# Performance work log

Measured on AMD Instinct MI355X. Metric: run time of the kernel, lower is better.

Reference implementation:

```python
import jax, jax.numpy as jnp
import numpy as np

BS, N, D, NE, NREL = 32, 512, 768, 64, 7


def setup_inputs() -> dict:
    key = jax.random.key(0)
    ks = jax.random.split(key, 8)
    bert_encoded = jax.random.normal(ks[0], (BS, N, D), dtype=jnp.float32)
    # variable-length spans [u, v) with 1 <= v-u <= 8, v <= N
    starts = jax.random.randint(ks[1], (BS, NE), 0, N - 8)
    lengths = jax.random.randint(ks[2], (BS, NE), 1, 9)
    ent_spans = jnp.stack([starts, starts + lengths], axis=-1).astype(jnp.int64)
    # some entities are padding (mask = 0), as in the original ne = max(len)
    ent_mask = (jax.random.uniform(ks[3], (BS, NE)) > 0.2).astype(jnp.float32)
    xav = (2.0 / (D + D)) ** 0.5  # xavier_normal std for square layers
    wq_w = jax.random.normal(ks[4], (D, D), dtype=jnp.float32) * xav
    wk_w = jax.random.normal(ks[5], (D, D), dtype=jnp.float32) * xav
    ln1_w = jax.random.normal(ks[6], (D, D), dtype=jnp.float32) * xav
    lno_w = jax.random.normal(ks[7], (NREL, D), dtype=jnp.float32) * (2.0 / (D + NREL)) ** 0.5
    return {
        "bert_encoded": bert_encoded,
        "ent_spans": ent_spans,
        "ent_mask": ent_mask,
        "wq_w": wq_w, "wq_b": jnp.zeros((D,), jnp.float32),
        "wk_w": wk_w, "wk_b": jnp.zeros((D,), jnp.float32),
        "ln1_w": ln1_w, "ln1_b": jnp.zeros((D,), jnp.float32),
        "lno_w": lno_w, "lno_b": jnp.zeros((NREL,), jnp.float32),
    }


def reference(bert_encoded, ent_spans, ent_mask,
              wq_w, wq_b, wk_w, wk_b, ln1_w, ln1_b, lno_w, lno_b):
    bs, n, d = bert_encoded.shape
    # span mean-pooling via exclusive-cumsum difference: mean over [u, v)
    cs = jnp.concatenate(
        [jnp.zeros((bs, 1, d), bert_encoded.dtype), jnp.cumsum(bert_encoded, axis=1)],
        axis=1)  # [bs, n+1, d]
    u = ent_spans[..., 0]  # [bs, ne]
    v = ent_spans[..., 1]
    cs_u = jnp.take_along_axis(cs, u[:, :, None], axis=1)  # [bs, ne, d]
    cs_v = jnp.take_along_axis(cs, v[:, :, None], axis=1)
    span_len = (v - u).astype(bert_encoded.dtype)[:, :, None]
    ent_encode = (cs_v - cs_u) / span_len
    # padded entities are zero vectors in the original (never written)
    ent_encode = ent_encode * ent_mask[:, :, None]
    # biaffine-style pairwise head (dropout = 0)
    q = jnp.einsum('bed,fd->bef', ent_encode, wq_w) + wq_b  # [bs, ne, d]
    k = jnp.einsum('bed,fd->bef', ent_encode, wk_w) + wk_b
    alpha = jax.nn.relu(q[:, :, None, :] + k[:, None, :, :])  # [bs, ne, ne, d]
    alpha = jax.nn.relu(jnp.einsum('bijd,ed->bije', alpha, ln1_w) + ln1_b)
    alpha = jnp.einsum('bijd,rd->bijr', alpha, lno_w) + lno_b  # [bs, ne, ne, nrel]
    alpha = alpha * ent_mask[:, :, None, None] * ent_mask[:, None, :, None]
    return alpha
```

## Files before the change

### kernel.cpp

```cpp
#include <hip/hip_runtime.h>
#include <hip/hip_bf16.h>

#define D 768
#define NE 64
#define BSZ 32
#define SEQ 512
#define NREL 7
#define NPAIR 131072
#define NEB 6

typedef __attribute__((ext_vector_type(8))) short short8;
typedef __attribute__((ext_vector_type(4))) float floatx4;

__device__ __forceinline__ short f2bf(float x) {
  union { __hip_bfloat16 b; short s; } u;
  u.b = __float2bfloat16(x);
  return u.s;
}

__device__ __forceinline__ float bf2f(short s) {
  return __uint_as_float(((unsigned)(unsigned short)s) << 16);
}

__device__ __forceinline__ void gl_lds16(const void* g, void* l) {
  __builtin_amdgcn_global_load_lds(
      (const __attribute__((address_space(1))) void*)g,
      (__attribute__((address_space(3))) void*)l, 16, 0, 0);
}

__global__ void __launch_bounds__(256) k_convert(const float* wq, const float* wk, const float* ln1,
                                                 short* owq, short* owk, short* oln1) {
  int idx = (blockIdx.x * 256 + threadIdx.x) * 4;
  if (idx >= D * D) return;
  float4 a = *(const float4*)(wq + idx);
  float4 b = *(const float4*)(wk + idx);
  float4 c = *(const float4*)(ln1 + idx);
  owq[idx + 0] = f2bf(a.x); owq[idx + 1] = f2bf(a.y); owq[idx + 2] = f2bf(a.z); owq[idx + 3] = f2bf(a.w);
  owk[idx + 0] = f2bf(b.x); owk[idx + 1] = f2bf(b.y); owk[idx + 2] = f2bf(b.z); owk[idx + 3] = f2bf(b.w);
  oln1[idx + 0] = f2bf(c.x); oln1[idx + 1] = f2bf(c.y); oln1[idx + 2] = f2bf(c.z); oln1[idx + 3] = f2bf(c.w);
}

__global__ void __launch_bounds__(256) k_pool(const float* bert, const int* spans, const float* mask,
                                              short* entb) {
  int be = blockIdx.x;
  int b = be >> 6;
  int u = spans[be * 2], v = spans[be * 2 + 1];
  float scale = mask[be] / (float)(v - u);
  const float* base = bert + (size_t)b * SEQ * D;
  for (int d = threadIdx.x; d < D; d += 256) {
    float s = 0.f;
    for (int t = u; t < v; ++t) s += base[t * D + d];
    entb[(size_t)be * D + d] = f2bf(s * scale);
  }
}

__global__ void __launch_bounds__(256) k_qk(const short* entb, const short* wqb, const short* wkb,
                                            const float* qbias, const float* kbias,
                                            short* qo, short* ko) {
  const int mblk = blockIdx.x, nblk = blockIdx.y;
  const short* W = blockIdx.z ? wkb : wqb;
  const float* bias = blockIdx.z ? kbias : qbias;
  short* out = blockIdx.z ? ko : qo;
  __shared__ __align__(16) char lds[32768];
  const int tid = threadIdx.x, wid = tid >> 6, lane = tid & 63;
  const int wm = wid >> 1, wn = wid & 1;
  floatx4 acc[4][4] = {};
  const int m0 = mblk * 128, n0 = nblk * 128;
  for (int kt = 0; kt < 12; ++kt) {
    const int d0 = kt * 64;
    __syncthreads();
#pragma unroll
    for (int is = 0; is < 4; ++is) {
      int lin = (wid * 4 + is) * 64 + lane;
      int row = lin >> 3, slot = lin & 7;
      int cg = slot ^ (row & 7);
      gl_lds16(entb + (size_t)(m0 + row) * D + d0 + cg * 8, lds + lin * 16);
    }
#pragma unroll
    for (int is = 0; is < 4; ++is) {
      int lin = (wid * 4 + is) * 64 + lane;
      int row = lin >> 3, slot = lin & 7;
      int cg = slot ^ (row & 7);
      gl_lds16(W + (size_t)(n0 + row) * D + d0 + cg * 8, lds + 16384 + lin * 16);
    }
    __syncthreads();
#pragma unroll
    for (int ks = 0; ks < 2; ++ks) {
      int kc = ks * 4 + (lane >> 4);
      short8 af[4], bf_[4];
#pragma unroll
      for (int m = 0; m < 4; ++m) {
        int row = wm * 64 + m * 16 + (lane & 15);
        af[m] = *(const short8*)(lds + row * 128 + ((kc ^ (row & 7)) << 4));
      }
#pragma unroll
      for (int n = 0; n < 4; ++n) {
        int row = wn * 64 + n * 16 + (lane & 15);
        bf_[n] = *(const short8*)(lds + 16384 + row * 128 + ((kc ^ (row & 7)) << 4));
      }
#pragma unroll
      for (int m = 0; m < 4; ++m)
#pragma unroll
        for (int n = 0; n < 4; ++n)
          acc[m][n] = __builtin_amdgcn_mfma_f32_16x16x32_bf16(af[m], bf_[n], acc[m][n], 0, 0, 0);
    }
  }
#pragma unroll
  for (int m = 0; m < 4; ++m)
#pragma unroll
    for (int rg = 0; rg < 4; ++rg) {
      int r = m0 + wm * 64 + m * 16 + ((lane >> 4) << 2) + rg;
#pragma unroll
      for (int n = 0; n < 4; ++n) {
        int c = n0 + wn * 64 + n * 16 + (lane & 15);
        out[(size_t)r * D + c] = f2bf(acc[m][n][rg] + bias[c]);
      }
    }
}

__global__ void __launch_bounds__(256, 3) k_main(const short* w1b, const short* qb, const short* kb,
                                                 const float* l1bias, const float* lno_w,
                                                 float* partial) {
  const int pblk = blockIdx.x, eblk = blockIdx.y;
  const int p0 = pblk * 128, e0 = eblk * 128;
  const int b = p0 >> 12, i0 = (p0 >> 6) & 63;
  __shared__ __align__(16) char lds[43264];
  const int tid = threadIdx.x, wid = tid >> 6, lane = tid & 63;
  const int wm = wid >> 1, wn = wid & 1;

  short* lnoT = (short*)(lds + 41216);
  for (int idx = tid; idx < 1024; idx += 256) {
    int e = idx >> 3, r = idx & 7;
    float v = (r < NREL) ? lno_w[r * D + e0 + e] : l1bias[e0 + e];
    lnoT[idx] = f2bf(v);
  }

  const int pl = tid >> 1;
  const int jj0 = pl & 63;
  const int qrow = 64 + (pl >> 6);
  const short* qbase = qb + (size_t)(b * NE + i0) * D;
  const short* kbase = kb + (size_t)(b * NE) * D;
  const int dpart = (tid & 1) * 32;

  floatx4 acc[4][4] = {};
  for (int kt = 0; kt < 12; ++kt) {
    const int d0 = kt * 64;
    __syncthreads();
#pragma unroll
    for (int is = 0; is < 4; ++is) {
      int c = is * 256 + tid;
      int row = c >> 3, sl = c & 7;
      int cg = sl ^ (row & 7);
      gl_lds16(w1b + (size_t)(e0 + row) * D + d0 + cg * 8, lds + c * 16);
    }
#pragma unroll
    for (int is = 0; is < 2; ++is) {
      int c = is * 256 + tid;
      int row = c >> 3, sl = c & 7;
      int cg = sl ^ (row & 7);
      gl_lds16(kbase + (size_t)row * D + d0 + cg * 8, lds + 32768 + c * 16);
    }
    if (tid < 16) {
      int row = 64 + (tid >> 3), sl = tid & 7;
      int cg = sl ^ (row & 7);
      gl_lds16(qbase + (size_t)(row - 64) * D + d0 + cg * 8,
               lds + 32768 + (512 + tid) * 16);
    }
    __syncthreads();
#pragma unroll
    for (int c4 = 0; c4 < 4; ++c4) {
      int cd = (dpart >> 3) + c4;
      short8 kv = *(const short8*)(lds + 32768 + jj0 * 128 + ((cd ^ (jj0 & 7)) << 4));
      short8 qv = *(const short8*)(lds + 32768 + qrow * 128 + ((cd ^ (qrow & 7)) << 4));
      short8 hv;
#pragma unroll
      for (int t = 0; t < 8; ++t)
        hv[t] = f2bf(fmaxf(bf2f(kv[t]) + bf2f(qv[t]), 0.f));
      int slot = cd ^ (pl & 7);
      *(short8*)(lds + 16384 + pl * 128 + (slot << 4)) = hv;
    }
    __syncthreads();
#pragma unroll
    for (int ks = 0; ks < 2; ++ks) {
      int kc = ks * 4 + (lane >> 4);
      short8 af[4], bf_[4];
#pragma unroll
      for (int m = 0; m < 4; ++m) {
        int row = wm * 64 + m * 16 + (lane & 15);
        af[m] = *(const short8*)(lds + row * 128 + ((kc ^ (row & 7)) << 4));
      }
#pragma unroll
      for (int n = 0; n < 4; ++n) {
        int row = wn * 64 + n * 16 + (lane & 15);
        bf_[n] = *(const short8*)(lds + 16384 + row * 128 + ((kc ^ (row & 7)) << 4));
      }
#pragma unroll
      for (int m = 0; m < 4; ++m)
#pragma unroll
        for (int n = 0; n < 4; ++n)
          acc[m][n] = __builtin_amdgcn_mfma_f32_16x16x32_bf16(af[m], bf_[n], acc[m][n], 0, 0, 0);
    }
  }

  float pr[4][NREL];
#pragma unroll
  for (int n = 0; n < 4; ++n)
#pragma unroll
    for (int r = 0; r < NREL; ++r) pr[n][r] = 0.f;
#pragma unroll
  for (int m = 0; m < 4; ++m)
#pragma unroll
    for (int rg = 0; rg < 4; ++rg) {
      int el = wm * 64 + m * 16 + ((lane >> 4) << 2) + rg;
      short8 wv = *(const short8*)(lnoT + el * 8);
      float w0 = bf2f(wv[0]), w1 = bf2f(wv[1]), w2 = bf2f(wv[2]), w3 = bf2f(wv[3]);
      float w4 = bf2f(wv[4]), w5 = bf2f(wv[5]), w6 = bf2f(wv[6]), bias = bf2f(wv[7]);
#pragma unroll
      for (int n = 0; n < 4; ++n) {
        float t = fmaxf(acc[m][n][rg] + bias, 0.f);
        pr[n][0] += t * w0; pr[n][1] += t * w1; pr[n][2] += t * w2; pr[n][3] += t * w3;
        pr[n][4] += t * w4; pr[n][5] += t * w5; pr[n][6] += t * w6;
      }
    }
#pragma unroll
  for (int n = 0; n < 4; ++n)
#pragma unroll
    for (int r = 0; r < NREL; ++r) {
      float v = pr[n][r];
      v += __shfl_xor(v, 16);
      v += __shfl_xor(v, 32);
      pr[n][r] = v;
    }

  __syncthreads();
  float* red = (float*)lds;
  if (wm == 1 && (lane >> 4) == 0) {
#pragma unroll
    for (int n = 0; n < 4; ++n) {
      float* dst = red + ((wn * 4 + n) * 16 + lane) * 8;
#pragma unroll
      for (int r = 0; r < NREL; ++r) dst[r] = pr[n][r];
    }
  }
  __syncthreads();
  if (wm == 0 && (lane >> 4) == 0) {
#pragma unroll
    for (int n = 0; n < 4; ++n) {
      const float* src = red + ((wn * 4 + n) * 16 + lane) * 8;
      int plc = wn * 64 + n * 16 + lane;
      int pg = p0 + plc;
      float4 o0, o1;
      o0.x = pr[n][0] + src[0]; o0.y = pr[n][1] + src[1];
      o0.z = pr[n][2] + src[2]; o0.w = pr[n][3] + src[3];
      o1.x = pr[n][4] + src[4]; o1.y = pr[n][5] + src[5];
      o1.z = pr[n][6] + src[6]; o1.w = 0.f;
      float4* dst = (float4*)(partial + ((size_t)eblk * NPAIR + pg) * 8);
      dst[0] = o0; dst[1] = o1;
    }
  }
}

__global__ void __launch_bounds__(256) k_reduce(const float* partial, const float* lno_b,
                                                const float* mask, float* out) {
  int pg = blockIdx.x * 256 + threadIdx.x;
  float s[7] = {0.f, 0.f, 0.f, 0.f, 0.f, 0.f, 0.f};
#pragma unroll
  for (int e = 0; e < NEB; ++e) {
    const float4* p = (const float4*)(partial + ((size_t)e * NPAIR + pg) * 8);
    float4 x0 = p[0], x1 = p[1];
    s[0] += x0.x; s[1] += x0.y; s[2] += x0.z; s[3] += x0.w;
    s[4] += x1.x; s[5] += x1.y; s[6] += x1.z;
  }
  int jj = pg & 63, ii = (pg >> 6) & 63, bb = pg >> 12;
  float f = mask[bb * NE + ii] * mask[bb * NE + jj];
#pragma unroll
  for (int r = 0; r < NREL; ++r) out[(size_t)pg * NREL + r] = (s[r] + lno_b[r]) * f;
}

extern "C" void kernel_launch(void* const* d_in, const int* in_sizes, int n_in,
                              void* d_out, int out_size, void* d_ws, size_t ws_size,
                              hipStream_t stream) {
  const float* bert = (const float*)d_in[0];
  const int* spans = (const int*)d_in[1];
  const float* mask = (const float*)d_in[2];
  const float* wq_w = (const float*)d_in[3];
  const float* wq_b = (const float*)d_in[4];
  const float* wk_w = (const float*)d_in[5];
  const float* wk_b = (const float*)d_in[6];
  const float* ln1_w = (const float*)d_in[7];
  const float* ln1_b = (const float*)d_in[8];
  const float* lno_w = (const float*)d_in[9];
  const float* lno_b = (const float*)d_in[10];
  float* out = (float*)d_out;
  char* ws = (char*)d_ws;

  short* entb  = (short*)(ws);
  short* wqb   = (short*)(ws + 3145728);
  short* wkb   = (short*)(ws + 4325376);
  short* ln1bf = (short*)(ws + 5505024);
  short* qbw   = (short*)(ws + 6684672);
  short* kbw   = (short*)(ws + 9830400);
  float* part  = (float*)(ws + 12976128);

  hipLaunchKernelGGL(k_convert, dim3(576), dim3(256), 0, stream, wq_w, wk_w, ln1_w, wqb, wkb, ln1bf);
  hipLaunchKernelGGL(k_pool, dim3(BSZ * NE), dim3(256), 0, stream, bert, spans, mask, entb);
  hipLaunchKernelGGL(k_qk, dim3(16, 6, 2), dim3(256), 0, stream, entb, wqb, wkb, wq_b, wk_b, qbw, kbw);
  hipLaunchKernelGGL(k_main, dim3(1024, NEB), dim3(256), 0, stream, ln1bf, qbw, kbw, ln1_b, lno_w, part);
  hipLaunchKernelGGL(k_reduce, dim3(NPAIR / 256), dim3(256), 0, stream, part, lno_b, mask, out);
}
```

Before: 356.5 us.

## Prefetch k tile during MFMA, keep q in fp32, pack bf16 relu with inline asm

```diff
diff --git a/kernel.cpp b/kernel.cpp
--- a/kernel.cpp
+++ b/kernel.cpp
@@ -16,10 +16,6 @@
   union { __hip_bfloat16 b; short s; } u;
   u.b = __float2bfloat16(x);
   return u.s;
-}
-
-__device__ __forceinline__ float bf2f(short s) {
-  return __uint_as_float(((unsigned)(unsigned short)s) << 16);
 }
 
 __device__ __forceinline__ void gl_lds16(const void* g, void* l) {
@@ -56,11 +52,10 @@
 
 __global__ void __launch_bounds__(256) k_qk(const short* entb, const short* wqb, const short* wkb,
                                             const float* qbias, const float* kbias,
-                                            short* qo, short* ko) {
+                                            float* qo, short* ko) {
   const int mblk = blockIdx.x, nblk = blockIdx.y;
   const short* W = blockIdx.z ? wkb : wqb;
   const float* bias = blockIdx.z ? kbias : qbias;
-  short* out = blockIdx.z ? ko : qo;
   __shared__ __align__(16) char lds[32768];
   const int tid = threadIdx.x, wid = tid >> 6, lane = tid & 63;
   const int wm = wid >> 1, wn = wid & 1;
@@ -113,39 +108,47 @@
 #pragma unroll
       for (int n = 0; n < 4; ++n) {
         int c = n0 + wn * 64 + n * 16 + (lane & 15);
-        out[(size_t)r * D + c] = f2bf(acc[m][n][rg] + bias[c]);
-      }
-    }
-}
-
-__global__ void __launch_bounds__(256, 3) k_main(const short* w1b, const short* qb, const short* kb,
+        float v = acc[m][n][rg] + bias[c];
+        if (blockIdx.z) ko[(size_t)r * D + c] = f2bf(v);
+        else            qo[(size_t)r * D + c] = v;
+      }
+    }
+}
+
+__global__ void __launch_bounds__(256, 3) k_main(const short* w1b, const float* qw, const short* kb,
                                                  const float* l1bias, const float* lno_w,
                                                  float* partial) {
   const int pblk = blockIdx.x, eblk = blockIdx.y;
   const int p0 = pblk * 128, e0 = eblk * 128;
   const int b = p0 >> 12, i0 = (p0 >> 6) & 63;
-  __shared__ __align__(16) char lds[43264];
+  __shared__ __align__(16) char lds[43008];
   const int tid = threadIdx.x, wid = tid >> 6, lane = tid & 63;
   const int wm = wid >> 1, wn = wid & 1;
 
-  short* lnoT = (short*)(lds + 41216);
+  short* lnoT = (short*)(lds + 40960);
   for (int idx = tid; idx < 1024; idx += 256) {
     int e = idx >> 3, r = idx & 7;
     float v = (r < NREL) ? lno_w[r * D + e0 + e] : l1bias[e0 + e];
     lnoT[idx] = f2bf(v);
   }
 
-  const int pl = tid >> 1;
-  const int jj0 = pl & 63;
-  const int qrow = 64 + (pl >> 6);
-  const short* qbase = qb + (size_t)(b * NE + i0) * D;
+  const float* qbase = qw + (size_t)(b * NE + i0) * D;
   const short* kbase = kb + (size_t)(b * NE) * D;
-  const int dpart = (tid & 1) * 32;
+  const int j2 = tid >> 2, dg = tid & 3;
 
   floatx4 acc[4][4] = {};
+
+#pragma unroll
+  for (int is = 0; is < 2; ++is) {
+    int c = is * 256 + tid;
+    int row = c >> 3, sl = c & 7;
+    int cg = sl ^ (row & 7);
+    gl_lds16(kbase + (size_t)row * D + cg * 8, lds + 32768 + c * 16);
+  }
+  __syncthreads();
+
   for (int kt = 0; kt < 12; ++kt) {
     const int d0 = kt * 64;
-    __syncthreads();
 #pragma unroll
     for (int is = 0; is < 4; ++is) {
       int c = is * 256 + tid;
@@ -153,33 +156,58 @@
       int cg = sl ^ (row & 7);
       gl_lds16(w1b + (size_t)(e0 + row) * D + d0 + cg * 8, lds + c * 16);
     }
-#pragma unroll
-    for (int is = 0; is < 2; ++is) {
-      int c = is * 256 + tid;
-      int row = c >> 3, sl = c & 7;
-      int cg = sl ^ (row & 7);
-      gl_lds16(kbase + (size_t)row * D + d0 + cg * 8, lds + 32768 + c * 16);
-    }
-    if (tid < 16) {
-      int row = 64 + (tid >> 3), sl = tid & 7;
-      int cg = sl ^ (row & 7);
-      gl_lds16(qbase + (size_t)(row - 64) * D + d0 + cg * 8,
-               lds + 32768 + (512 + tid) * 16);
+    short8 kv0 = *(const short8*)(lds + 32768 + j2 * 128 + ((((dg * 2)) ^ (j2 & 7)) << 4));
+    short8 kv1 = *(const short8*)(lds + 32768 + j2 * 128 + ((((dg * 2 + 1)) ^ (j2 & 7)) << 4));
+    union { short8 s; unsigned u[4]; } K0, K1;
+    K0.s = kv0; K1.s = kv1;
+    float kf[16];
+#pragma unroll
+    for (int t = 0; t < 4; ++t) {
+      kf[2 * t]     = __uint_as_float(K0.u[t] << 16);
+      kf[2 * t + 1] = __uint_as_float(K0.u[t] & 0xFFFF0000u);
+      kf[8 + 2 * t]     = __uint_as_float(K1.u[t] << 16);
+      kf[8 + 2 * t + 1] = __uint_as_float(K1.u[t] & 0xFFFF0000u);
+    }
+#pragma unroll
+    for (int r = 0; r < 2; ++r) {
+      const float* qp = qbase + (size_t)r * D + d0 + dg * 16;
+      floatx4 qa = *(const floatx4*)(qp);
+      floatx4 qb2 = *(const floatx4*)(qp + 4);
+      floatx4 qc = *(const floatx4*)(qp + 8);
+      floatx4 qd = *(const floatx4*)(qp + 12);
+      float qf[16];
+#pragma unroll
+      for (int t = 0; t < 4; ++t) {
+        qf[t] = qa[t]; qf[4 + t] = qb2[t]; qf[8 + t] = qc[t]; qf[12 + t] = qd[t];
+      }
+      unsigned w[8];
+#pragma unroll
+      for (int t = 0; t < 8; ++t) {
+        float lo = qf[2 * t] + kf[2 * t];
+        float hi = qf[2 * t + 1] + kf[2 * t + 1];
+        unsigned cw, rw;
+        asm("v_cvt_pk_bf16_f32 %0, %1, %2" : "=v"(cw) : "v"(lo), "v"(hi));
+        asm("v_pk_max_i16 %0, %1, 0" : "=v"(rw) : "v"(cw));
+        w[t] = rw;
+      }
+      int hrow = r * 64 + j2;
+      union { unsigned u[4]; short8 s; } W0, W1;
+      W0.u[0] = w[0]; W0.u[1] = w[1]; W0.u[2] = w[2]; W0.u[3] = w[3];
+      W1.u[0] = w[4]; W1.u[1] = w[5]; W1.u[2] = w[6]; W1.u[3] = w[7];
+      *(short8*)(lds + 16384 + hrow * 128 + (((dg * 2) ^ (j2 & 7)) << 4)) = W0.s;
+      *(short8*)(lds + 16384 + hrow * 128 + (((dg * 2 + 1) ^ (j2 & 7)) << 4)) = W1.s;
     }
     __syncthreads();
-#pragma unroll
-    for (int c4 = 0; c4 < 4; ++c4) {
-      int cd = (dpart >> 3) + c4;
-      short8 kv = *(const short8*)(lds + 32768 + jj0 * 128 + ((cd ^ (jj0 & 7)) << 4));
-      short8 qv = *(const short8*)(lds + 32768 + qrow * 128 + ((cd ^ (qrow & 7)) << 4));
-      short8 hv;
-#pragma unroll
-      for (int t = 0; t < 8; ++t)
-        hv[t] = f2bf(fmaxf(bf2f(kv[t]) + bf2f(qv[t]), 0.f));
-      int slot = cd ^ (pl & 7);
-      *(short8*)(lds + 16384 + pl * 128 + (slot << 4)) = hv;
-    }
-    __syncthreads();
+    if (kt < 11) {
+      const int d1 = d0 + 64;
+#pragma unroll
+      for (int is = 0; is < 2; ++is) {
+        int c = is * 256 + tid;
+        int row = c >> 3, sl = c & 7;
+        int cg = sl ^ (row & 7);
+        gl_lds16(kbase + (size_t)row * D + d1 + cg * 8, lds + 32768 + c * 16);
+      }
+    }
 #pragma unroll
     for (int ks = 0; ks < 2; ++ks) {
       int kc = ks * 4 + (lane >> 4);
@@ -200,6 +228,7 @@
         for (int n = 0; n < 4; ++n)
           acc[m][n] = __builtin_amdgcn_mfma_f32_16x16x32_bf16(af[m], bf_[n], acc[m][n], 0, 0, 0);
     }
+    __syncthreads();
   }
 
   float pr[4][NREL];
@@ -213,8 +242,14 @@
     for (int rg = 0; rg < 4; ++rg) {
       int el = wm * 64 + m * 16 + ((lane >> 4) << 2) + rg;
       short8 wv = *(const short8*)(lnoT + el * 8);
-      float w0 = bf2f(wv[0]), w1 = bf2f(wv[1]), w2 = bf2f(wv[2]), w3 = bf2f(wv[3]);
-      float w4 = bf2f(wv[4]), w5 = bf2f(wv[5]), w6 = bf2f(wv[6]), bias = bf2f(wv[7]);
+      float w0 = __uint_as_float(((unsigned)(unsigned short)wv[0]) << 16);
+      float w1 = __uint_as_float(((unsigned)(unsigned short)wv[1]) << 16);
+      float w2 = __uint_as_float(((unsigned)(unsigned short)wv[2]) << 16);
+      float w3 = __uint_as_float(((unsigned)(unsigned short)wv[3]) << 16);
+      float w4 = __uint_as_float(((unsigned)(unsigned short)wv[4]) << 16);
+      float w5 = __uint_as_float(((unsigned)(unsigned short)wv[5]) << 16);
+      float w6 = __uint_as_float(((unsigned)(unsigned short)wv[6]) << 16);
+      float bias = __uint_as_float(((unsigned)(unsigned short)wv[7]) << 16);
 #pragma unroll
       for (int n = 0; n < 4; ++n) {
         float t = fmaxf(acc[m][n][rg] + bias, 0.f);
@@ -298,13 +333,13 @@
   short* wqb   = (short*)(ws + 3145728);
   short* wkb   = (short*)(ws + 4325376);
   short* ln1bf = (short*)(ws + 5505024);
-  short* qbw   = (short*)(ws + 6684672);
-  short* kbw   = (short*)(ws + 9830400);
-  float* part  = (float*)(ws + 12976128);
+  float* qw    = (float*)(ws + 6684672);
+  short* kbw   = (short*)(ws + 12976128);
+  float* part  = (float*)(ws + 16121856);
 
   hipLaunchKernelGGL(k_convert, dim3(576), dim3(256), 0, stream, wq_w, wk_w, ln1_w, wqb, wkb, ln1bf);
   hipLaunchKernelGGL(k_pool, dim3(BSZ * NE), dim3(256), 0, stream, bert, spans, mask, entb);
-  hipLaunchKernelGGL(k_qk, dim3(16, 6, 2), dim3(256), 0, stream, entb, wqb, wkb, wq_b, wk_b, qbw, kbw);
-  hipLaunchKernelGGL(k_main, dim3(1024, NEB), dim3(256), 0, stream, ln1bf, qbw, kbw, ln1_b, lno_w, part);
+  hipLaunchKernelGGL(k_qk, dim3(16, 6, 2), dim3(256), 0, stream, entb, wqb, wkb, wq_b, wk_b, qw, kbw);
+  hipLaunchKernelGGL(k_main, dim3(1024, NEB), dim3(256), 0, stream, ln1bf, qw, kbw, ln1_b, lno_w, part);
   hipLaunchKernelGGL(k_reduce, dim3(NPAIR / 256), dim3(256), 0, stream, part, lno_b, mask, out);
 }
```

Result: slower. 389.9 us (+9.4%).
